# Optimization experiments

Measured on AMD Instinct MI355X. Metric: run time of the kernel, lower is better.

Reference implementation:

```python
import jax, jax.numpy as jnp
import numpy as np

DT = 0.001  # fixed dt in SimplifiedSSM.forward
LN_EPS = 1e-5


def _layernorm(x, g, b):
    m = jnp.mean(x, axis=-1, keepdims=True)
    v = jnp.mean(jnp.square(x - m), axis=-1, keepdims=True)
    return (x - m) * jax.lax.rsqrt(v + LN_EPS) * g + b


def setup_inputs() -> dict:
    key = jax.random.key(0)
    ks = jax.random.split(key, 12)
    Bn, C, H, W = 8, 1024, 32, 32
    depth, S = 4, 128
    d = C
    inp = {
        "x": jax.random.normal(ks[0], (Bn, C, H, W), dtype=jnp.float32),
        # SSM params, stacked over depth. A scaled by 0.1 for numerical stability
        # of the length-1024 recurrence (same math, tamer eigenvalues).
        "A": 0.1 * jax.random.normal(ks[1], (depth, S, S), dtype=jnp.float32),
        "Bp": jax.random.normal(ks[2], (depth, S, d), dtype=jnp.float32),
        "Cp": jax.random.normal(ks[3], (depth, d, S), dtype=jnp.float32),
        "Dp": jax.random.normal(ks[4], (depth, d), dtype=jnp.float32),
        # Linear layers (PyTorch convention: y = x @ W.T + b)
        "Wi": jax.random.normal(ks[5], (depth, d, d), dtype=jnp.float32) / np.sqrt(d),
        "bi": jax.random.normal(ks[6], (depth, d), dtype=jnp.float32) * 0.01,
        "Wo": jax.random.normal(ks[7], (depth, d, d), dtype=jnp.float32) / np.sqrt(d),
        "bo": jax.random.normal(ks[8], (depth, d), dtype=jnp.float32) * 0.01,
        # LayerNorm affine params
        "gamma": jnp.ones((depth, d), dtype=jnp.float32),
        "beta": jnp.zeros((depth, d), dtype=jnp.float32),
    }
    return inp


def reference(x, A, Bp, Cp, Dp, Wi, bi, Wo, bo, gamma, beta):
    Bn, C, H, W = x.shape
    depth, S, _ = A.shape
    # b c h w -> b (h w) c
    seq = x.reshape(Bn, C, H * W).transpose(0, 2, 1)
    eye = jnp.eye(S, dtype=x.dtype)
    for i in range(depth):
        n = _layernorm(seq, gamma[i], beta[i])
        u = n @ Wi[i].T + bi[i]                       # (B, L, d)
        A_bar = eye + DT * A[i]                       # (S, S)
        ub = jnp.einsum('bld,sd->lbs', u, DT * Bp[i]) # (L, B, S)

        def step(h, ub_t):
            h = h @ A_bar.T + ub_t
            return h, h

        h0 = jnp.zeros((Bn, S), dtype=x.dtype)
        _, hs = jax.lax.scan(step, h0, ub)            # hs: (L, B, S)
        y = jnp.einsum('lbs,ds->bld', hs, Cp[i]) + u * Dp[i]
        seq = seq + y @ Wo[i].T + bo[i]
    return seq.transpose(0, 2, 1).reshape(Bn, C, H, W)
```

## Files before the change

### kernel.cpp

```cpp
#include <hip/hip_runtime.h>
#include <stdint.h>

#define DT_STEP 0.001f
#define LN_EPS  1e-5f
#define Bn      8
#define Lseq    1024
#define Dm      1024
#define Sn      128
#define DEPTH   4
#define Mrows   (Bn * Lseq)
#define Qc      32
#define NCHUNK  (Lseq / Qc)
#define NPOW    33

typedef short bf16x8 __attribute__((ext_vector_type(8)));
typedef float f32x4  __attribute__((ext_vector_type(4)));

__device__ __forceinline__ unsigned short f2bf(float f) {
    unsigned int u = __float_as_uint(f);
    u += 0x7fffu + ((u >> 16) & 1u);
    return (unsigned short)(u >> 16);
}

#define GLOAD_LDS16(gp, lp)                                                \
    __builtin_amdgcn_global_load_lds(                                      \
        (const __attribute__((address_space(1))) unsigned int*)(gp),       \
        (__attribute__((address_space(3))) unsigned int*)(lp), 16, 0, 0)

__global__ __launch_bounds__(256) void f2bf_kernel(const float* __restrict__ src,
                                                   unsigned short* __restrict__ dst,
                                                   int n) {
    int i = (blockIdx.x * 256 + threadIdx.x) * 4;
    if (i < n) {
        float4 v = *(const float4*)(src + i);
        ushort4 o;
        o.x = f2bf(v.x); o.y = f2bf(v.y); o.z = f2bf(v.z); o.w = f2bf(v.w);
        *(ushort4*)(dst + i) = o;
    }
}

__global__ __launch_bounds__(256) void convscale_kernel(const float* __restrict__ Wo,
                                                        const float* __restrict__ Dp,
                                                        unsigned short* __restrict__ dst) {
    int z = blockIdx.y;
    int i = (blockIdx.x * 256 + threadIdx.x) * 4;
    const float* S = Wo + (size_t)z * Dm * Dm;
    const float* dp = Dp + (size_t)z * Dm;
    float4 v = *(const float4*)(S + i);
    int c = i & (Dm - 1);
    float4 d = *(const float4*)(dp + c);
    ushort4 o;
    o.x = f2bf(v.x * d.x); o.y = f2bf(v.y * d.y);
    o.z = f2bf(v.z * d.z); o.w = f2bf(v.w * d.w);
    *(ushort4*)(dst + (size_t)z * Dm * Dm + i) = o;
}

__global__ __launch_bounds__(256) void transpose_f2bf(const float* __restrict__ src,
                                                      unsigned short* __restrict__ dst,
                                                      int R, int C) {
    __shared__ float t[32][33];
    int z = blockIdx.z;
    const float* S = src + (size_t)z * R * C;
    unsigned short* D = dst + (size_t)z * R * C;
    int r0 = blockIdx.y * 32, c0 = blockIdx.x * 32;
    int tx = threadIdx.x & 31, ty = threadIdx.x >> 5;
    for (int rr = ty; rr < 32; rr += 8)
        t[rr][tx] = S[(size_t)(r0 + rr) * C + c0 + tx];
    __syncthreads();
    for (int rr = ty; rr < 32; rr += 8)
        D[(size_t)(c0 + rr) * R + r0 + tx] = f2bf(t[tx][rr]);
}

__global__ __launch_bounds__(256) void c2dt_kernel(const float* __restrict__ Bp,
                                                   const float* __restrict__ bi,
                                                   float* __restrict__ c2dt) {
    int z = blockIdx.x, s = blockIdx.y;
    int tid = threadIdx.x;
    const float* br = Bp + ((size_t)z * Sn + s) * Dm;
    const float* bb = bi + (size_t)z * Dm;
    float4 v = *(const float4*)(br + tid * 4);
    float4 w = *(const float4*)(bb + tid * 4);
    float acc = v.x * w.x + v.y * w.y + v.z * w.z + v.w * w.w;
#pragma unroll
    for (int off = 32; off > 0; off >>= 1) acc += __shfl_down(acc, off, 64);
    __shared__ float red[4];
    if ((tid & 63) == 0) red[tid >> 6] = acc;
    __syncthreads();
    if (tid == 0) c2dt[z * Sn + s] = DT_STEP * (red[0] + red[1] + red[2] + red[3]);
}

__global__ __launch_bounds__(1024) void transpose_bll(const float* __restrict__ src,
                                                      float* __restrict__ dst) {
    __shared__ float tile[32][33];
    int b  = blockIdx.z;
    int i0 = blockIdx.y * 32, j0 = blockIdx.x * 32;
    int tx = threadIdx.x, ty = threadIdx.y;
    const float* S = src + (size_t)b * Dm * Lseq;
    float*       D = dst + (size_t)b * Dm * Lseq;
    tile[ty][tx] = S[(size_t)(j0 + ty) * 1024 + i0 + tx];
    __syncthreads();
    D[(size_t)(i0 + ty) * 1024 + j0 + tx] = tile[tx][ty];
}

__global__ __launch_bounds__(256) void ln_kernel(const float* __restrict__ x,
                                                 unsigned short* __restrict__ outp,
                                                 const float* __restrict__ g,
                                                 const float* __restrict__ bta) {
    int row = blockIdx.x;
    int tid = threadIdx.x;
    const float* xr = x + (size_t)row * Dm;
    float4 v = *(const float4*)(xr + tid * 4);
    float s  = v.x + v.y + v.z + v.w;
    float ss = v.x * v.x + v.y * v.y + v.z * v.z + v.w * v.w;
#pragma unroll
    for (int off = 32; off > 0; off >>= 1) {
        s  += __shfl_down(s, off, 64);
        ss += __shfl_down(ss, off, 64);
    }
    __shared__ float red[8];
    __shared__ float mv[2];
    int wave = tid >> 6, lane = tid & 63;
    if (lane == 0) { red[wave] = s; red[4 + wave] = ss; }
    __syncthreads();
    if (tid == 0) {
        float st  = red[0] + red[1] + red[2] + red[3];
        float sst = red[4] + red[5] + red[6] + red[7];
        float mean = st / (float)Dm;
        float var  = sst / (float)Dm - mean * mean;
        mv[0] = mean;
        mv[1] = rsqrtf(var + LN_EPS);
    }
    __syncthreads();
    float mean = mv[0], rstd = mv[1];
    int c = tid * 4;
    float4 gv = *(const float4*)(g + c);
    float4 bv = *(const float4*)(bta + c);
    ushort4 o;
    o.x = f2bf((v.x - mean) * rstd * gv.x + bv.x);
    o.y = f2bf((v.y - mean) * rstd * gv.y + bv.y);
    o.z = f2bf((v.z - mean) * rstd * gv.z + bv.z);
    o.w = f2bf((v.w - mean) * rstd * gv.w + bv.w);
    *(ushort4*)(outp + (size_t)row * Dm + c) = o;
}

__global__ __launch_bounds__(512) void gemm_bk64(
    const unsigned short* __restrict__ A1, int sA1,
    const unsigned short* __restrict__ A2, int sA2, int KA1,
    const unsigned short* __restrict__ B1, int sB1,
    const unsigned short* __restrict__ B2, int sB2,
    float* __restrict__ Cf, unsigned short* __restrict__ Ch,
    const float* __restrict__ bias1, const float* __restrict__ bias2,
    int ny, int N, int K, float scale, int mode,
    long batchA, long batchB, long batchC) {
    __shared__ __align__(16) unsigned short As[1024 * 8];
    __shared__ __align__(16) unsigned short Bs[1024 * 8];
    int flat = blockIdx.x;
    int rb = flat % ny, cb = flat / ny;
    int row0 = rb * 128, col0 = cb * 128;
    int z = blockIdx.y;
    int tid  = threadIdx.x;
    int wave = tid >> 6, lane = tid & 63;
    int wm = (wave & 1) * 64, wn = (wave >> 1) * 32;
    int lr = lane & 15, lq = lane >> 4;

    int rowS[2], kclS[2], slotOff[2];
#pragma unroll
    for (int q = 0; q < 2; q++) {
        int s = tid + q * 512;
        rowS[q] = s >> 3;
        kclS[q] = (s & 7) ^ ((s >> 3) & 7);
        slotOff[q] = s * 8;
    }
    int aoff[4][2], boff[2][2];
#pragma unroll
    for (int i = 0; i < 4; i++)
#pragma unroll
        for (int h = 0; h < 2; h++) {
            int ra = wm + i * 16 + lr;
            aoff[i][h] = (ra * 8 + ((lq + 4 * h) ^ (ra & 7))) * 8;
        }
#pragma unroll
    for (int j = 0; j < 2; j++)
#pragma unroll
        for (int h = 0; h < 2; h++) {
            int rn = wn + j * 16 + lr;
            boff[j][h] = (rn * 8 + ((lq + 4 * h) ^ (rn & 7))) * 8;
        }

    const unsigned short* A1b = A1 + (size_t)z * batchA;
    const unsigned short* BfixBlk = nullptr;
    int sBfix = sB1;
    if (mode == 0) {
        if (col0 < N - 128) { BfixBlk = B1 + (size_t)col0 * sB1; sBfix = sB1; }
        else                { BfixBlk = B2;                      sBfix = sB2; }
    } else if (mode == 2) {
        BfixBlk = B1 + (size_t)z * batchB + (size_t)col0 * sB1;
        sBfix = sB1;
    }

    f32x4 acc[4][2];
#pragma unroll
    for (int i = 0; i < 4; i++)
#pragma unroll
        for (int j = 0; j < 2; j++) acc[i][j] = (f32x4){0.f, 0.f, 0.f, 0.f};

    for (int k0 = 0; k0 < K; k0 += 64) {
        const unsigned short *Ab, *Bb;
        int sa, sb, ko;
        if (mode == 1) {
            if (k0 < KA1) { Ab = A1; sa = sA1; Bb = B1 + (size_t)col0 * sB1; sb = sB1; ko = k0; }
            else          { Ab = A2; sa = sA2; Bb = B2 + (size_t)col0 * sB2; sb = sB2; ko = k0 - KA1; }
        } else {
            Ab = A1b; sa = sA1; Bb = BfixBlk; sb = sBfix; ko = k0;
        }
        const unsigned short* Abr = Ab + (size_t)row0 * sa + ko;
        const unsigned short* Bbr = Bb + ko;
        __syncthreads();
#pragma unroll
        for (int q = 0; q < 2; q++) {
            GLOAD_LDS16(Abr + (size_t)rowS[q] * sa + kclS[q] * 8, &As[slotOff[q]]);
            GLOAD_LDS16(Bbr + (size_t)rowS[q] * sb + kclS[q] * 8, &Bs[slotOff[q]]);
        }
        __syncthreads();
#pragma unroll
        for (int h = 0; h < 2; h++) {
            bf16x8 af[4], bfr[2];
#pragma unroll
            for (int i = 0; i < 4; i++) af[i]  = *(const bf16x8*)&As[aoff[i][h]];
#pragma unroll
            for (int j = 0; j < 2; j++) bfr[j] = *(const bf16x8*)&Bs[boff[j][h]];
#pragma unroll
            for (int i = 0; i < 4; i++)
#pragma unroll
                for (int j = 0; j < 2; j++)
                    acc[i][j] = __builtin_amdgcn_mfma_f32_16x16x32_bf16(af[i], bfr[j],
                                                                       acc[i][j], 0, 0, 0);
        }
    }
#pragma unroll
    for (int i = 0; i < 4; i++) {
#pragma unroll
        for (int j = 0; j < 2; j++) {
#pragma unroll
            for (int r = 0; r < 4; r++) {
                int row = row0 + wm + i * 16 + lq * 4 + r;
                int col = col0 + wn + j * 16 + lr;
                float v = acc[i][j][r];
                if (mode == 0) {
                    int nu = N - 128;
                    if (col < nu) {
                        Ch[(size_t)row * nu + col] = f2bf(v + bias1[col]);
                    } else {
                        int cc = col - nu;
                        Cf[(size_t)row * 128 + cc] = v + bias2[cc];
                    }
                } else if (mode == 1) {
                    size_t idx = (size_t)row * N + col;
                    Cf[idx] = Cf[idx] + v + bias1[col];
                } else {
                    Ch[(size_t)z * batchC + (size_t)row * N + col] = f2bf(v * scale);
                }
            }
        }
    }
}

__global__ __launch_bounds__(128) void pow_init(const float* __restrict__ Amat,
                                                float* __restrict__ Pow) {
    int i = blockIdx.x;
    int s = blockIdx.y;
    int k = threadIdx.x;
    float eye = (s == k) ? 1.f : 0.f;
    size_t base = (size_t)i * NPOW * (Sn * Sn);
    Pow[base + (size_t)s * Sn + k] = eye;
    Pow[base + (size_t)(Sn * Sn) + (size_t)s * Sn + k] =
        eye + DT_STEP * Amat[(size_t)i * Sn * Sn + (size_t)s * Sn + k];
}

__global__ __launch_bounds__(256) void pow_mul(float* __restrict__ Pow, int m, int kmax) {
    int job = blockIdx.z;
    int i  = job / kmax;
    int kk = job % kmax + 1;
    const float* Pa = Pow + ((size_t)i * NPOW + m) * (Sn * Sn);
    const float* Pb = Pow + ((size_t)i * NPOW + kk) * (Sn * Sn);
    float*       Pc = Pow + ((size_t)i * NPOW + m + kk) * (Sn * Sn);
    int r0 = blockIdx.y * 64, c0 = blockIdx.x * 32;
    __shared__ float Asl[64 * 129];
    __shared__ float Bsl[128 * 32];
    int tx = threadIdx.x, ty = threadIdx.y;
    int tid = ty * 16 + tx;
    for (int idx = tid; idx < 64 * 128; idx += 256) {
        int r = idx >> 7, cc = idx & 127;
        Asl[r * 129 + cc] = Pa[(size_t)(r0 + r) * 128 + cc];
    }
    for (int idx = tid; idx < 128 * 32; idx += 256) {
        int r = idx >> 5, cc = idx & 31;
        Bsl[r * 32 + cc] = Pb[(size_t)r * 128 + c0 + cc];
    }
    __syncthreads();
    float acc[4][2] = {{0.f,0.f},{0.f,0.f},{0.f,0.f},{0.f,0.f}};
    for (int k = 0; k < 128; k++) {
        float b0 = Bsl[k * 32 + tx * 2];
        float b1 = Bsl[k * 32 + tx * 2 + 1];
#pragma unroll
        for (int r = 0; r < 4; r++) {
            float a = Asl[(ty * 4 + r) * 129 + k];
            acc[r][0] += a * b0;
            acc[r][1] += a * b1;
        }
    }
#pragma unroll
    for (int r = 0; r < 4; r++) {
        Pc[(size_t)(r0 + ty * 4 + r) * 128 + c0 + tx * 2]     = acc[r][0];
        Pc[(size_t)(r0 + ty * 4 + r) * 128 + c0 + tx * 2 + 1] = acc[r][1];
    }
}

__global__ __launch_bounds__(128) void local_scan(const float* __restrict__ ub,
                                                  float* __restrict__ hs,
                                                  const float* __restrict__ Abar) {
    int b = blockIdx.x / NCHUNK;
    int c = blockIdx.x % NCHUNK;
    int s = threadIdx.x;
    float arow[Sn];
#pragma unroll
    for (int k = 0; k < Sn; k += 4) {
        float4 v = *(const float4*)(Abar + (size_t)s * Sn + k);
        arow[k] = v.x; arow[k + 1] = v.y; arow[k + 2] = v.z; arow[k + 3] = v.w;
    }
    __shared__ __align__(16) float hsh[Sn];
    hsh[s] = 0.f;
    __syncthreads();
    size_t base = (size_t)(b * Lseq + c * Qc) * Sn + s;
    for (int t = 0; t < Qc; t++) {
        float ut = ub[base + (size_t)t * Sn];
        float a0 = 0.f, a1 = 0.f, a2 = 0.f, a3 = 0.f;
#pragma unroll
        for (int k = 0; k < Sn; k += 16) {
            float4 h0 = *(const float4*)&hsh[k];
            float4 h1 = *(const float4*)&hsh[k + 4];
            float4 h2 = *(const float4*)&hsh[k + 8];
            float4 h3 = *(const float4*)&hsh[k + 12];
            a0 += arow[k + 0] * h0.x + arow[k + 1] * h0.y + arow[k + 2] * h0.z + arow[k + 3] * h0.w;
            a1 += arow[k + 4] * h1.x + arow[k + 5] * h1.y + arow[k + 6] * h1.z + arow[k + 7] * h1.w;
            a2 += arow[k + 8] * h2.x + arow[k + 9] * h2.y + arow[k + 10] * h2.z + arow[k + 11] * h2.w;
            a3 += arow[k + 12] * h3.x + arow[k + 13] * h3.y + arow[k + 14] * h3.z + arow[k + 15] * h3.w;
        }
        float hv = ut + (a0 + a1) + (a2 + a3);
        hs[base + (size_t)t * Sn] = hv;
        __syncthreads();
        hsh[s] = hv;
        __syncthreads();
    }
}

__global__ __launch_bounds__(128) void carry_scan(const float* __restrict__ hs,
                                                  const float* __restrict__ AQ,
                                                  float* __restrict__ carry) {
    int b = blockIdx.x;
    int s = threadIdx.x;
    float le[NCHUNK];
#pragma unroll
    for (int c = 0; c < NCHUNK; c++)
        le[c] = hs[(size_t)(b * Lseq + c * Qc + Qc - 1) * Sn + s];
    float arow[Sn];
#pragma unroll
    for (int k = 0; k < Sn; k += 4) {
        float4 v = *(const float4*)(AQ + (size_t)s * Sn + k);
        arow[k] = v.x; arow[k + 1] = v.y; arow[k + 2] = v.z; arow[k + 3] = v.w;
    }
    __shared__ __align__(16) float csh[Sn];
    csh[s] = 0.f;
    __syncthreads();
    for (int c = 0; c < NCHUNK; c++) {
        carry[((size_t)b * NCHUNK + c) * Sn + s] = csh[s];
        float a0 = 0.f, a1 = 0.f, a2 = 0.f, a3 = 0.f;
#pragma unroll
        for (int k = 0; k < Sn; k += 16) {
            float4 h0 = *(const float4*)&csh[k];
            float4 h1 = *(const float4*)&csh[k + 4];
            float4 h2 = *(const float4*)&csh[k + 8];
            float4 h3 = *(const float4*)&csh[k + 12];
            a0 += arow[k + 0] * h0.x + arow[k + 1] * h0.y + arow[k + 2] * h0.z + arow[k + 3] * h0.w;
            a1 += arow[k + 4] * h1.x + arow[k + 5] * h1.y + arow[k + 6] * h1.z + arow[k + 7] * h1.w;
            a2 += arow[k + 8] * h2.x + arow[k + 9] * h2.y + arow[k + 10] * h2.z + arow[k + 11] * h2.w;
            a3 += arow[k + 12] * h3.x + arow[k + 13] * h3.y + arow[k + 14] * h3.z + arow[k + 15] * h3.w;
        }
        float cv = le[c] + (a0 + a1) + (a2 + a3);
        __syncthreads();
        csh[s] = cv;
        __syncthreads();
    }
}

__global__ __launch_bounds__(256) void fixup_scan(const float* __restrict__ hs,
                                                  unsigned short* __restrict__ hs_bf,
                                                  const float* __restrict__ PowLayer,
                                                  const float* __restrict__ carry) {
    int t  = blockIdx.x;
    int c4 = blockIdx.y;
    const float* P = PowLayer + (size_t)(t + 1) * (Sn * Sn);
    __shared__ float Pl[Sn * 65];
    __shared__ float cl[4][Bn * Sn];
    int tid = threadIdx.x;
#pragma unroll
    for (int cc = 0; cc < 4; cc++)
        for (int idx = tid; idx < Bn * Sn; idx += 256)
            cl[cc][idx] = carry[((size_t)(idx >> 7) * NCHUNK + (c4 * 4 + cc)) * Sn + (idx & 127)];
    int s = tid & 127, bh = tid >> 7;
    float acc[4][4];
#pragma unroll
    for (int cc = 0; cc < 4; cc++)
#pragma unroll
        for (int j = 0; j < 4; j++) acc[cc][j] = 0.f;
    for (int kh = 0; kh < 2; kh++) {
        __syncthreads();
        for (int idx = tid; idx < Sn * 64; idx += 256) {
            int r = idx >> 6, kk = idx & 63;
            Pl[r * 65 + kk] = P[(size_t)r * Sn + kh * 64 + kk];
        }
        __syncthreads();
        for (int kk = 0; kk < 64; kk++) {
            float pw = Pl[s * 65 + kk];
            int kg = kh * 64 + kk;
#pragma unroll
            for (int cc = 0; cc < 4; cc++)
#pragma unroll
                for (int j = 0; j < 4; j++)
                    acc[cc][j] += pw * cl[cc][(bh * 4 + j) * Sn + kg];
        }
    }
#pragma unroll
    for (int cc = 0; cc < 4; cc++) {
        int c = c4 * 4 + cc;
#pragma unroll
        for (int j = 0; j < 4; j++) {
            int bb = bh * 4 + j;
            size_t rowi = (size_t)(bb * Lseq + c * Qc + t) * Sn + s;
            hs_bf[rowi] = f2bf(hs[rowi] + acc[cc][j]);
        }
    }
}

extern "C" void kernel_launch(void* const* d_in, const int* in_sizes, int n_in,
                              void* d_out, int out_size, void* d_ws, size_t ws_size,
                              hipStream_t stream) {
    const float* x     = (const float*)d_in[0];
    const float* Am    = (const float*)d_in[1];
    const float* Bp    = (const float*)d_in[2];
    const float* Cp    = (const float*)d_in[3];
    const float* Dp    = (const float*)d_in[4];
    const float* Wi    = (const float*)d_in[5];
    const float* bi    = (const float*)d_in[6];
    const float* Wo    = (const float*)d_in[7];
    const float* bo    = (const float*)d_in[8];
    const float* gamma = (const float*)d_in[9];
    const float* beta  = (const float*)d_in[10];
    float* out = (float*)d_out;
    (void)in_sizes; (void)n_in; (void)out_size; (void)ws_size;

    char* ws = (char*)d_ws;
    float*          seq   = (float*)(ws + (size_t)0);
    unsigned short* nbuf  = (unsigned short*)(ws + (size_t)33554432);
    unsigned short* WiTh  = (unsigned short*)(ws + (size_t)33554432);
    unsigned short* Woh   = (unsigned short*)(ws + (size_t)41943040);
    unsigned short* u     = (unsigned short*)(ws + (size_t)50331648);
    float*          ub    = (float*)(ws + (size_t)67108864);
    float*          hs    = (float*)(ws + (size_t)71303168);
    unsigned short* hs_bf = (unsigned short*)(ws + (size_t)75497472);
    float*          Pow   = (float*)(ws + (size_t)77594624);
    float*          carry = (float*)(ws + (size_t)86245376);
    unsigned short* Wih   = (unsigned short*)(ws + (size_t)86376448);
    unsigned short* Wo2h  = (unsigned short*)(ws + (size_t)94765056);
    unsigned short* Bph   = (unsigned short*)(ws + (size_t)103153664);
    unsigned short* CpTh  = (unsigned short*)(ws + (size_t)104202240);
    unsigned short* M2h   = (unsigned short*)(ws + (size_t)105250816);
    unsigned short* W3h   = (unsigned short*)(ws + (size_t)106299392);
    float*          c2dt  = (float*)(ws + (size_t)107347968);

    const long WW = (long)Dm * Dm;
    const long SW = (long)Sn * Dm;

    hipLaunchKernelGGL(f2bf_kernel, dim3(DEPTH * WW / 1024), dim3(256), 0, stream,
                       Wi, Wih, DEPTH * (int)WW);
    hipLaunchKernelGGL(f2bf_kernel, dim3(DEPTH * WW / 1024), dim3(256), 0, stream,
                       Wo, Woh, DEPTH * (int)WW);
    hipLaunchKernelGGL(f2bf_kernel, dim3(DEPTH * SW / 1024), dim3(256), 0, stream,
                       Bp, Bph, DEPTH * (int)SW);
    hipLaunchKernelGGL(convscale_kernel, dim3(WW / 1024, DEPTH), dim3(256), 0, stream,
                       Wo, Dp, Wo2h);
    hipLaunchKernelGGL(transpose_f2bf, dim3(32, 32, DEPTH), dim3(256), 0, stream,
                       Wi, WiTh, Dm, Dm);
    hipLaunchKernelGGL(transpose_f2bf, dim3(4, 32, DEPTH), dim3(256), 0, stream,
                       Cp, CpTh, Dm, Sn);
    hipLaunchKernelGGL(c2dt_kernel, dim3(DEPTH, Sn), dim3(256), 0, stream, Bp, bi, c2dt);

    hipLaunchKernelGGL(gemm_bk64, dim3(8, DEPTH), dim3(512), 0, stream,
                       Bph, Dm, (const unsigned short*)nullptr, 0, 0,
                       WiTh, Dm, (const unsigned short*)nullptr, 0,
                       (float*)nullptr, M2h, (const float*)nullptr, (const float*)nullptr,
                       1, Dm, Dm, DT_STEP, 2, SW, WW, SW);
    hipLaunchKernelGGL(gemm_bk64, dim3(8, DEPTH), dim3(512), 0, stream,
                       Woh, Dm, (const unsigned short*)nullptr, 0, 0,
                       CpTh, Dm, (const unsigned short*)nullptr, 0,
                       (float*)nullptr, W3h, (const float*)nullptr, (const float*)nullptr,
                       8, Sn, Dm, 1.f, 2, WW, SW, SW);

    hipLaunchKernelGGL(transpose_bll, dim3(32, 32, Bn), dim3(32, 32), 0, stream, x, seq);

    hipLaunchKernelGGL(pow_init, dim3(DEPTH, Sn), dim3(Sn), 0, stream, Am, Pow);
    for (int m = 1; m < Qc; m <<= 1) {
        hipLaunchKernelGGL(pow_mul, dim3(4, 2, DEPTH * m), dim3(16, 16), 0, stream,
                           Pow, m, m);
    }

    for (int i = 0; i < DEPTH; i++) {
        const unsigned short* Wi_i  = Wih  + (size_t)i * WW;
        const unsigned short* Wo2_i = Wo2h + (size_t)i * WW;
        const unsigned short* M2_i  = M2h  + (size_t)i * SW;
        const unsigned short* W3_i  = W3h  + (size_t)i * SW;
        const float* PowL = Pow + (size_t)i * NPOW * (Sn * Sn);

        hipLaunchKernelGGL(ln_kernel, dim3(Mrows), dim3(256), 0, stream,
                           seq, nbuf, gamma + i * Dm, beta + i * Dm);
        hipLaunchKernelGGL(gemm_bk64, dim3(9 * 64, 1), dim3(512), 0, stream,
                           nbuf, Dm, (const unsigned short*)nullptr, 0, 0,
                           Wi_i, Dm, M2_i, Dm,
                           ub, u, bi + i * Dm, c2dt + i * Sn,
                           64, Dm + Sn, Dm, 1.f, 0, 0, 0, 0);
        hipLaunchKernelGGL(local_scan, dim3(Bn * NCHUNK), dim3(Sn), 0, stream,
                           ub, hs, PowL + (size_t)1 * Sn * Sn);
        hipLaunchKernelGGL(carry_scan, dim3(Bn), dim3(Sn), 0, stream,
                           hs, PowL + (size_t)Qc * Sn * Sn, carry);
        hipLaunchKernelGGL(fixup_scan, dim3(Qc, NCHUNK / 4), dim3(256), 0, stream,
                           hs, hs_bf, PowL, carry);
        hipLaunchKernelGGL(gemm_bk64, dim3(8 * 64, 1), dim3(512), 0, stream,
                           hs_bf, Sn, u, Dm, Sn,
                           W3_i, Sn, Wo2_i, Dm,
                           seq, (unsigned short*)nullptr, bo + i * Dm, (const float*)nullptr,
                           64, Dm, Dm + Sn, 1.f, 1, 0, 0, 0);
    }

    hipLaunchKernelGGL(transpose_bll, dim3(32, 32, Bn), dim3(32, 32), 0, stream, seq, out);
}
```

Measured before the change: 812.4 us.

## Fold the Wi projection into a precomputed Wo·diag(Dp)·Wi product

The skip path u*Dp passes through Wo, so Wo·diag(Dp)·Wi is precomputed once per layer as a combined weight W4, with the bias term folded into an effective output bias. The per-layer first GEMM then only produces the 128-wide ub columns instead of the full 1024+128 u output, and the output GEMM reads the layernormed activations directly. This removes a large M×1024×1024 GEMM per layer and the u write and read, at the cost of one extra weight-product GEMM at setup and a change in bf16 rounding order.

```diff
diff --git a/kernel.cpp b/kernel.cpp
--- a/kernel.cpp
+++ b/kernel.cpp
@@ -87,6 +87,30 @@
     if ((tid & 63) == 0) red[tid >> 6] = acc;
     __syncthreads();
     if (tid == 0) c2dt[z * Sn + s] = DT_STEP * (red[0] + red[1] + red[2] + red[3]);
+}
+
+__global__ __launch_bounds__(256) void boeff_kernel(const float* __restrict__ Wo,
+                                                    const float* __restrict__ Dp,
+                                                    const float* __restrict__ bi,
+                                                    const float* __restrict__ bo,
+                                                    float* __restrict__ boeff) {
+    int z = blockIdx.x, c = blockIdx.y;
+    int tid = threadIdx.x;
+    const float* wr = Wo + ((size_t)z * Dm + c) * Dm;
+    const float* dp = Dp + (size_t)z * Dm;
+    const float* bb = bi + (size_t)z * Dm;
+    float4 w = *(const float4*)(wr + tid * 4);
+    float4 d = *(const float4*)(dp + tid * 4);
+    float4 b = *(const float4*)(bb + tid * 4);
+    float acc = w.x * d.x * b.x + w.y * d.y * b.y + w.z * d.z * b.z + w.w * d.w * b.w;
+#pragma unroll
+    for (int off = 32; off > 0; off >>= 1) acc += __shfl_down(acc, off, 64);
+    __shared__ float red[4];
+    if ((tid & 63) == 0) red[tid >> 6] = acc;
+    __syncthreads();
+    if (tid == 0)
+        boeff[(size_t)z * Dm + c] =
+            bo[(size_t)z * Dm + c] + red[0] + red[1] + red[2] + red[3];
 }
 
 __global__ __launch_bounds__(1024) void transpose_bll(const float* __restrict__ src,
@@ -464,13 +488,13 @@
     unsigned short* nbuf  = (unsigned short*)(ws + (size_t)33554432);
     unsigned short* WiTh  = (unsigned short*)(ws + (size_t)33554432);
     unsigned short* Woh   = (unsigned short*)(ws + (size_t)41943040);
-    unsigned short* u     = (unsigned short*)(ws + (size_t)50331648);
+    unsigned short* W4h   = (unsigned short*)(ws + (size_t)50331648);
+    float*          boeff = (float*)(ws + (size_t)58720256);
     float*          ub    = (float*)(ws + (size_t)67108864);
     float*          hs    = (float*)(ws + (size_t)71303168);
     unsigned short* hs_bf = (unsigned short*)(ws + (size_t)75497472);
     float*          Pow   = (float*)(ws + (size_t)77594624);
     float*          carry = (float*)(ws + (size_t)86245376);
-    unsigned short* Wih   = (unsigned short*)(ws + (size_t)86376448);
     unsigned short* Wo2h  = (unsigned short*)(ws + (size_t)94765056);
     unsigned short* Bph   = (unsigned short*)(ws + (size_t)103153664);
     unsigned short* CpTh  = (unsigned short*)(ws + (size_t)104202240);
@@ -481,8 +505,6 @@
     const long WW = (long)Dm * Dm;
     const long SW = (long)Sn * Dm;
 
-    hipLaunchKernelGGL(f2bf_kernel, dim3(DEPTH * WW / 1024), dim3(256), 0, stream,
-                       Wi, Wih, DEPTH * (int)WW);
     hipLaunchKernelGGL(f2bf_kernel, dim3(DEPTH * WW / 1024), dim3(256), 0, stream,
                        Wo, Woh, DEPTH * (int)WW);
     hipLaunchKernelGGL(f2bf_kernel, dim3(DEPTH * SW / 1024), dim3(256), 0, stream,
@@ -494,6 +516,8 @@
     hipLaunchKernelGGL(transpose_f2bf, dim3(4, 32, DEPTH), dim3(256), 0, stream,
                        Cp, CpTh, Dm, Sn);
     hipLaunchKernelGGL(c2dt_kernel, dim3(DEPTH, Sn), dim3(256), 0, stream, Bp, bi, c2dt);
+    hipLaunchKernelGGL(boeff_kernel, dim3(DEPTH, Dm), dim3(256), 0, stream,
+                       Wo, Dp, bi, bo, boeff);
 
     hipLaunchKernelGGL(gemm_bk64, dim3(8, DEPTH), dim3(512), 0, stream,
                        Bph, Dm, (const unsigned short*)nullptr, 0, 0,
@@ -505,6 +529,11 @@
                        CpTh, Dm, (const unsigned short*)nullptr, 0,
                        (float*)nullptr, W3h, (const float*)nullptr, (const float*)nullptr,
                        8, Sn, Dm, 1.f, 2, WW, SW, SW);
+    hipLaunchKernelGGL(gemm_bk64, dim3(8 * 8, DEPTH), dim3(512), 0, stream,
+                       Wo2h, Dm, (const unsigned short*)nullptr, 0, 0,
+                       WiTh, Dm, (const unsigned short*)nullptr, 0,
+                       (float*)nullptr, W4h, (const float*)nullptr, (const float*)nullptr,
+                       8, Dm, Dm, 1.f, 2, WW, WW, WW);
 
     hipLaunchKernelGGL(transpose_bll, dim3(32, 32, Bn), dim3(32, 32), 0, stream, x, seq);
 
@@ -515,19 +544,18 @@
     }
 
     for (int i = 0; i < DEPTH; i++) {
-        const unsigned short* Wi_i  = Wih  + (size_t)i * WW;
-        const unsigned short* Wo2_i = Wo2h + (size_t)i * WW;
-        const unsigned short* M2_i  = M2h  + (size_t)i * SW;
-        const unsigned short* W3_i  = W3h  + (size_t)i * SW;
+        const unsigned short* M2_i = M2h + (size_t)i * SW;
+        const unsigned short* W3_i = W3h + (size_t)i * SW;
+        const unsigned short* W4_i = W4h + (size_t)i * WW;
         const float* PowL = Pow + (size_t)i * NPOW * (Sn * Sn);
 
         hipLaunchKernelGGL(ln_kernel, dim3(Mrows), dim3(256), 0, stream,
                            seq, nbuf, gamma + i * Dm, beta + i * Dm);
-        hipLaunchKernelGGL(gemm_bk64, dim3(9 * 64, 1), dim3(512), 0, stream,
+        hipLaunchKernelGGL(gemm_bk64, dim3(64, 1), dim3(512), 0, stream,
                            nbuf, Dm, (const unsigned short*)nullptr, 0, 0,
-                           Wi_i, Dm, M2_i, Dm,
-                           ub, u, bi + i * Dm, c2dt + i * Sn,
-                           64, Dm + Sn, Dm, 1.f, 0, 0, 0, 0);
+                           (const unsigned short*)nullptr, 0, M2_i, Dm,
+                           ub, (unsigned short*)nullptr, bi + i * Dm, c2dt + i * Sn,
+                           64, Sn, Dm, 1.f, 0, 0, 0, 0);
         hipLaunchKernelGGL(local_scan, dim3(Bn * NCHUNK), dim3(Sn), 0, stream,
                            ub, hs, PowL + (size_t)1 * Sn * Sn);
         hipLaunchKernelGGL(carry_scan, dim3(Bn), dim3(Sn), 0, stream,
@@ -535,9 +563,9 @@
         hipLaunchKernelGGL(fixup_scan, dim3(Qc, NCHUNK / 4), dim3(256), 0, stream,
                            hs, hs_bf, PowL, carry);
         hipLaunchKernelGGL(gemm_bk64, dim3(8 * 64, 1), dim3(512), 0, stream,
-                           hs_bf, Sn, u, Dm, Sn,
-                           W3_i, Sn, Wo2_i, Dm,
-                           seq, (unsigned short*)nullptr, bo + i * Dm, (const float*)nullptr,
+                           hs_bf, Sn, nbuf, Dm, Sn,
+                           W3_i, Sn, W4_i, Dm,
+                           seq, (unsigned short*)nullptr, boeff + i * Dm, (const float*)nullptr,
                            64, Dm, Dm + Sn, 1.f, 1, 0, 0, 0);
     }
 
```

Result: no change. 810.7 us (-0.2%).
